# Kernel optimization log

Measured on AMD Instinct MI355X. Metric: run time of the kernel, lower is better.

The kernel has to match this reference:

```python
import jax, jax.numpy as jnp
import numpy as np

B, T, D, H = 2, 2048, 2048, 16
DK = D // H  # 128
THETA = 10000.0


def _rope_angles():
    inv_freq = 1.0 / (THETA ** (np.arange(0, DK, 2, dtype=np.float32) / DK))  # (DK/2,)
    pos = np.arange(T, dtype=np.float32)
    freqs = pos[:, None] * inv_freq[None, :]  # (T, DK/2)
    return jnp.asarray(np.broadcast_to(freqs[None], (B, T, DK // 2)).copy())


def setup_inputs() -> dict:
    key = jax.random.key(0)
    k1, k2, k3 = jax.random.split(key, 3)
    x = jax.random.normal(k1, (B, T, D), dtype=jnp.float32)
    Wqkv = jax.random.normal(k2, (D, 3 * D), dtype=jnp.float32) * (D ** -0.5)
    Wout = jax.random.normal(k3, (D, D), dtype=jnp.float32) * (D ** -0.5)
    return {"x": x, "freqs": _rope_angles(), "Wqkv": Wqkv, "Wout": Wout}


def _apply_rope(xh, cos, sin):
    # xh: (B,T,H,DK); consecutive pairs form complex numbers (torch view_as_complex)
    xr = xh[..., 0::2]  # (B,T,H,DK/2) real parts
    xi = xh[..., 1::2]  # imag parts
    # cos/sin: (B,T,1,DK/2)
    or_ = xr * cos - xi * sin
    oi_ = xr * sin + xi * cos
    return jnp.stack([or_, oi_], axis=-1).reshape(xh.shape)


def reference(x, freqs, Wqkv, Wout):
    qkv = x @ Wqkv  # (B,T,3D)
    qkv = qkv.reshape(B, T, H, 3 * DK)
    q, k, v = qkv[..., :DK], qkv[..., DK:2 * DK], qkv[..., 2 * DK:]
    cos = jnp.cos(freqs)[:, :, None, :]
    sin = jnp.sin(freqs)[:, :, None, :]
    q = _apply_rope(q, cos, sin)
    k = _apply_rope(k, cos, sin)
    # (B,H,T,DK)
    q = q.transpose(0, 2, 1, 3)
    k = k.transpose(0, 2, 1, 3)
    v = v.transpose(0, 2, 1, 3)
    scores = jnp.einsum('bhqd,bhkd->bhqk', q, k) * (DK ** -0.5)
    causal = jnp.tril(jnp.ones((T, T), dtype=bool))
    scores = jnp.where(causal[None, None], scores, -jnp.inf)
    attn = jax.nn.softmax(scores, axis=-1)
    attn = jnp.nan_to_num(attn)
    out = jnp.einsum('bhqk,bhkd->bhqd', attn, v)  # (B,H,T,DK)
    out = out.transpose(0, 2, 1, 3).reshape(B, T, D)
    return out @ Wout
```

## Files before the change

kernel.cpp:

```cpp
#include <hip/hip_runtime.h>
#include <cstdint>

#define BATCH   2
#define T_SEQ   2048
#define NH      16
#define DK      128
#define DMODEL  2048
#define NQKV    6144

using short8 = __attribute__((ext_vector_type(8))) short;
using f32x4  = __attribute__((ext_vector_type(4))) float;
using f32x16 = __attribute__((ext_vector_type(16))) float;

__device__ __forceinline__ float bf2f(unsigned short u) {
    union { float f; uint32_t i; } x; x.i = ((uint32_t)u) << 16; return x.f;
}
__device__ __forceinline__ unsigned short f2bf(float f) {
    union { float f; uint32_t i; } x; x.f = f;
    uint32_t r = x.i + 0x7fffu + ((x.i >> 16) & 1u);
    return (unsigned short)(r >> 16);
}

__device__ __forceinline__ void async_load16(const unsigned short* g, unsigned short* l) {
    __builtin_amdgcn_global_load_lds(
        (const __attribute__((address_space(1))) unsigned int*)g,
        (__attribute__((address_space(3))) unsigned int*)l,
        16, 0, 0);
}


__global__ void cast_x_kernel(const float* __restrict__ x,
                              unsigned short* __restrict__ xb, int n4) {
    int i = blockIdx.x * 256 + threadIdx.x;
    if (i >= n4) return;
    float4 v = ((const float4*)x)[i];
    ushort4 o;
    o.x = f2bf(v.x); o.y = f2bf(v.y); o.z = f2bf(v.z); o.w = f2bf(v.w);
    ((ushort4*)xb)[i] = o;
}

__global__ void wtrans_kernel(const float* __restrict__ W,
                              unsigned short* __restrict__ WT, int K, int N) {
    __shared__ unsigned short tile[64][65];
    int k0 = blockIdx.y * 64, n0 = blockIdx.x * 64;
    for (int it = 0; it < 16; ++it) {
        int idx = it * 256 + threadIdx.x;
        int r = idx >> 6, c = idx & 63;
        tile[r][c] = f2bf(W[(size_t)(k0 + r) * N + n0 + c]);
    }
    __syncthreads();
    for (int it = 0; it < 16; ++it) {
        int idx = it * 256 + threadIdx.x;
        int r = idx >> 6, c = idx & 63;
        WT[(size_t)(n0 + r) * K + k0 + c] = tile[c][r];
    }
}

template <int MODE>
__global__ __launch_bounds__(256) void gemm_bt_kernel(
    const unsigned short* __restrict__ A, const unsigned short* __restrict__ BT,
    float* __restrict__ Cout,
    unsigned short* __restrict__ qraw, unsigned short* __restrict__ kraw,
    unsigned short* __restrict__ vtb,
    int M, int N, int K) {
    __shared__ __align__(16) unsigned short As[128 * 64];
    __shared__ __align__(16) unsigned short Bs[128 * 64];
    const int tid = threadIdx.x;
    const int w = tid >> 6, lane = tid & 63;
    const int l31 = lane & 31, lhi = lane >> 5;
    const int m0 = blockIdx.y * 128, n0 = blockIdx.x * 128;
    const int wm = (w & 1) * 64, wn = (w >> 1) * 64;

    f32x16 acc[2][2];
#pragma unroll
    for (int a = 0; a < 2; ++a)
#pragma unroll
        for (int b = 0; b < 2; ++b)
#pragma unroll
            for (int r = 0; r < 16; ++r) acc[a][b][r] = 0.f;

    for (int k0 = 0; k0 < K; k0 += 64) {
#pragma unroll
        for (int j = 0; j < 4; ++j) {
            int c   = (w * 4 + j) * 64 + lane;
            int row = c >> 3;
            int kcg = (c & 7) ^ (row & 7);
            async_load16(A  + (size_t)(m0 + row) * K + k0 + kcg * 8,
                         As + (size_t)(w * 4 + j) * 64 * 8);
            async_load16(BT + (size_t)(n0 + row) * K + k0 + kcg * 8,
                         Bs + (size_t)(w * 4 + j) * 64 * 8);
        }
        __syncthreads();
#pragma unroll
        for (int ks = 0; ks < 4; ++ks) {
            short8 af[2], bfr[2];
#pragma unroll
            for (int mt = 0; mt < 2; ++mt) {
                int row = wm + mt * 32 + l31;
                int kcs = (ks * 2 + lhi) ^ (row & 7);
                af[mt] = *(const short8*)(As + row * 64 + kcs * 8);
            }
#pragma unroll
            for (int nt = 0; nt < 2; ++nt) {
                int row = wn + nt * 32 + l31;
                int kcs = (ks * 2 + lhi) ^ (row & 7);
                bfr[nt] = *(const short8*)(Bs + row * 64 + kcs * 8);
            }
#pragma unroll
            for (int mt = 0; mt < 2; ++mt)
#pragma unroll
                for (int nt = 0; nt < 2; ++nt)
                    acc[mt][nt] = __builtin_amdgcn_mfma_f32_32x32x16_bf16(
                        af[mt], bfr[nt], acc[mt][nt], 0, 0, 0);
        }
        __syncthreads();
    }

    if (MODE == 0) {
#pragma unroll
        for (int mt = 0; mt < 2; ++mt)
#pragma unroll
            for (int nt = 0; nt < 2; ++nt)
#pragma unroll
                for (int r = 0; r < 16; ++r) {
                    int row = m0 + wm + mt * 32 + (r & 3) + 8 * (r >> 2) + 4 * lhi;
                    int col = n0 + wn + nt * 32 + l31;
                    Cout[(size_t)row * N + col] = acc[mt][nt][r];
                }
    }
}

#define G1_K 2048
#define G1_N 6144

__global__ __launch_bounds__(512, 2) void gemm8p_qkv_kernel(
    const unsigned short* __restrict__ A, const unsigned short* __restrict__ BT,
    unsigned short* __restrict__ qraw, unsigned short* __restrict__ kraw,
    unsigned short* __restrict__ vtb) {
    __shared__ __align__(16) unsigned short As[2][256 * 64];
    __shared__ __align__(16) unsigned short Bs[2][256 * 64];

    const int tid = threadIdx.x;
    const int w = tid >> 6, lane = tid & 63;
    const int l15 = lane & 15, quad = lane >> 4, l7 = lane & 7;
    const int wm = (w & 1) * 128, wn = (w >> 1) * 64;

    const int id = blockIdx.x;
    const int wg = (id & 7) * 48 + (id >> 3);
    const int by = wg / 24, bx = wg - by * 24;
    const int m0 = by * 256, n0 = bx * 256;

    const int r64 = tid >> 3;
    const int csw = (tid & 7) ^ (r64 & 7);

    auto stageA = [&](int buf, int kt, int h) {
#pragma unroll
        for (int j = 0; j < 2; ++j) {
            const int rg = h * 64 + j * 128 + r64;
            async_load16(A + (size_t)(m0 + rg) * G1_K + kt * 64 + csw * 8,
                         &As[buf][(h * 64 + j * 128 + w * 8) << 6]);
        }
    };
    auto stageB = [&](int buf, int kt, int h) {
#pragma unroll
        for (int j = 0; j < 2; ++j) {
            const int rbw = j * 128 + ((w >> 2) << 6) + h * 32 + ((w & 3) << 3);
            const int rg  = rbw + (lane >> 3);
            async_load16(BT + (size_t)(n0 + rg) * G1_K + kt * 64 + csw * 8,
                         &Bs[buf][rbw << 6]);
        }
    };

    f32x4 acc[8][4];
#pragma unroll
    for (int i = 0; i < 8; ++i)
#pragma unroll
        for (int j = 0; j < 4; ++j) acc[i][j] = (f32x4){0.f, 0.f, 0.f, 0.f};

#define LOADA(BUF, H)                                                           \
  _Pragma("unroll") for (int mt = 0; mt < 4; ++mt)                              \
    _Pragma("unroll") for (int ks = 0; ks < 2; ++ks)                            \
      paf[mt][ks] = *(const short8*)(&As[BUF][((wm + (H)*64 + mt*16 + l15)      \
          << 6) + (((ks*4 + quad) ^ l7) << 3)]);

#define LOADB(BUF, H, DST)                                                      \
  _Pragma("unroll") for (int nt = 0; nt < 2; ++nt)                              \
    _Pragma("unroll") for (int ks = 0; ks < 2; ++ks)                            \
      DST[nt][ks] = *(const short8*)(&Bs[BUF][((wn + (H)*32 + nt*16 + l15)      \
          << 6) + (((ks*4 + quad) ^ l7) << 3)]);

#define MFMAQ(QM, QN, PB)                                                       \
  __builtin_amdgcn_s_setprio(1);                                                \
  _Pragma("unroll") for (int mt = 0; mt < 4; ++mt)                              \
    _Pragma("unroll") for (int nt = 0; nt < 2; ++nt)                            \
      _Pragma("unroll") for (int ks = 0; ks < 2; ++ks)                          \
        acc[(QM)*4 + mt][(QN)*2 + nt] =                                         \
            __builtin_amdgcn_mfma_f32_16x16x32_bf16(                            \
                paf[mt][ks], PB[nt][ks], acc[(QM)*4 + mt][(QN)*2 + nt],         \
                0, 0, 0);                                                       \
  __builtin_amdgcn_s_setprio(0);

#define LGK0 asm volatile("s_waitcnt lgkmcnt(0)" ::: "memory");                 \
             __builtin_amdgcn_sched_barrier(0)
#define LGK8 asm volatile("s_waitcnt lgkmcnt(8)" ::: "memory")
#define BAR  __builtin_amdgcn_s_barrier()
#define VM4  asm volatile("s_waitcnt vmcnt(4)" ::: "memory")
#define VM0  asm volatile("s_waitcnt vmcnt(0)" ::: "memory")

    stageA(0, 0, 0); stageB(0, 0, 0); stageA(0, 0, 1); stageB(0, 0, 1);
    stageA(1, 1, 0); stageB(1, 1, 0);
    VM4;
    BAR;

    const int NI = G1_K / 128;
    for (int it = 0; it < NI; ++it) {
        const int t1 = 2 * it + 1;
        const bool last = (it == NI - 1);
        short8 paf[4][2], pbf0[2][2], pbf1[2][2];
        LOADA(0, 0) LOADB(0, 0, pbf0)
        stageA(1, t1, 1);
        LGK8; BAR; LGK0;
        MFMAQ(0, 0, pbf0)
        BAR;
        LOADB(0, 1, pbf1)
        stageB(1, t1, 1);
        BAR; LGK0;
        MFMAQ(0, 1, pbf1)
        BAR;
        LOADA(0, 1)
        if (!last) stageA(0, t1 + 1, 0);
        BAR; LGK0;
        MFMAQ(1, 1, pbf1)
        BAR;
        if (!last) stageB(0, t1 + 1, 0);
        BAR;
        MFMAQ(1, 0, pbf0)
        if (last) { VM0; } else { VM4; }
        BAR;
        LOADA(1, 0) LOADB(1, 0, pbf0)
        if (!last) stageA(0, t1 + 1, 1);
        LGK8; BAR; LGK0;
        MFMAQ(0, 0, pbf0)
        BAR;
        LOADB(1, 1, pbf1)
        if (!last) stageB(0, t1 + 1, 1);
        BAR; LGK0;
        MFMAQ(0, 1, pbf1)
        BAR;
        LOADA(1, 1)
        if (!last) stageA(1, t1 + 2, 0);
        BAR; LGK0;
        MFMAQ(1, 1, pbf1)
        BAR;
        if (!last) stageB(1, t1 + 2, 0);
        BAR;
        MFMAQ(1, 0, pbf0)
        if (!last) { VM4; }
        BAR;
    }

#pragma unroll
    for (int i8 = 0; i8 < 8; ++i8) {
        const int grow0 = m0 + wm + i8 * 16 + quad * 4;
        const int bi = grow0 >> 11;
        const int tb = grow0 & (T_SEQ - 1);
#pragma unroll
        for (int j4 = 0; j4 < 4; ++j4) {
            const int gcol = n0 + wn + j4 * 16 + l15;
            const int h   = gcol / 384;
            const int r3  = gcol - h * 384;
            const int sec = r3 >> 7;
            const int dk  = r3 & 127;
            if (sec < 2) {
                unsigned short* dst = (sec == 0 ? qraw : kraw) +
                    ((size_t)(bi * NH + h) * T_SEQ + tb) * DK + dk;
#pragma unroll
                for (int r = 0; r < 4; ++r)
                    dst[(size_t)r * DK] = f2bf(acc[i8][j4][r]);
            } else {
                unsigned short* dst = vtb +
                    ((size_t)(bi * NH + h) * DK + dk) * T_SEQ + tb;
                ushort4 p;
                p.x = f2bf(acc[i8][j4][0]); p.y = f2bf(acc[i8][j4][1]);
                p.z = f2bf(acc[i8][j4][2]); p.w = f2bf(acc[i8][j4][3]);
                *(ushort4*)dst = p;
            }
        }
    }
#undef LOADA
#undef LOADB
#undef MFMAQ
#undef LGK0
#undef LGK8
#undef BAR
#undef VM4
#undef VM0
}

__global__ void rope_kernel(unsigned short* __restrict__ qraw,
                            unsigned short* __restrict__ kraw,
                            const float* __restrict__ freqs) {
    int linear = blockIdx.x * 256 + threadIdx.x;
    int i  = linear & 63;
    int t  = (linear >> 6) & (T_SEQ - 1);
    int bh = linear >> 17;
    int b  = bh >> 4;
    float f  = freqs[((size_t)b * T_SEQ + t) * 64 + i];
    float cs = __cosf(f), sn = __sinf(f);
    size_t off = ((size_t)bh * T_SEQ + t) * DK + 2 * i;
    ushort2 qp = *(ushort2*)(qraw + off);
    ushort2 kp = *(ushort2*)(kraw + off);
    float qr = bf2f(qp.x), qi = bf2f(qp.y);
    float kr = bf2f(kp.x), ki = bf2f(kp.y);
    ushort2 qo, ko;
    qo.x = f2bf(qr * cs - qi * sn); qo.y = f2bf(qr * sn + qi * cs);
    ko.x = f2bf(kr * cs - ki * sn); ko.y = f2bf(kr * sn + ki * cs);
    *(ushort2*)(qraw + off) = qo;
    *(ushort2*)(kraw + off) = ko;
}

__global__ __launch_bounds__(256) void attn_kernel(
    const unsigned short* __restrict__ qb, const unsigned short* __restrict__ kb,
    const unsigned short* __restrict__ vt, unsigned short* __restrict__ ctx) {
    __shared__ __align__(16) unsigned short Ks[2][64 * 128];
    __shared__ __align__(16) unsigned short Vs[2][128 * 64];
    __shared__ __align__(16) unsigned short pbuf[4][16 * 68];
    const int qt   = 31 - blockIdx.y;
    const int u    = blockIdx.x;
    const int bh   = ((u & 7) << 2) | (u >> 3);
    const int q0   = qt * 64;
    const int w    = threadIdx.x >> 6, lane = threadIdx.x & 63;
    const int lrow = lane & 15, quad = lane >> 4;
    const int qrow = q0 + w * 16;
    const float sc2 = 0.08838834764831845f * 1.4426950408889634f;
    const short8 vone = {16256, 16256, 16256, 16256, 16256, 16256, 16256, 16256};

    short8 aq[4];
    const unsigned short* qbase = qb + ((size_t)bh * T_SEQ + qrow + lrow) * DK;
#pragma unroll
    for (int kk = 0; kk < 4; ++kk)
        aq[kk] = *(const short8*)(qbase + kk * 32 + quad * 8);

    f32x4 o[8];
#pragma unroll
    for (int d = 0; d < 8; ++d) o[d] = (f32x4){0.f, 0.f, 0.f, 0.f};
    f32x4 ol = (f32x4){0.f, 0.f, 0.f, 0.f};

    const unsigned short* kg0 = kb + (size_t)bh * T_SEQ * DK;
    const unsigned short* vg0 = vt + (size_t)bh * DK * T_SEQ;

    auto stage = [&](int kt, int sbuf) {
        const unsigned short* kg = kg0 + (size_t)kt * 64 * DK;
        const unsigned short* vg = vg0 + kt * 64;
        unsigned short* Kd = &Ks[sbuf][0];
        unsigned short* Vd = &Vs[sbuf][0];
#pragma unroll
        for (int j = 0; j < 4; ++j) {
            int c = (w * 4 + j) * 64 + lane;
            int kr_ = c >> 4, kc = (c & 15) ^ (kr_ & 7);
            async_load16(kg + (size_t)kr_ * DK + kc * 8, Kd + c * 8);
            int vr = c >> 3, vc = (c & 7) ^ (vr & 7);
            async_load16(vg + (size_t)vr * T_SEQ + vc * 8, Vd + c * 8);
        }
    };

    stage(0, 0);
    for (int kt = 0; kt <= qt; ++kt) {
        __syncthreads();
        if (kt < qt) stage(kt + 1, (kt + 1) & 1);
        const unsigned short* Kb = &Ks[kt & 1][0];
        const unsigned short* Vb = &Vs[kt & 1][0];

        f32x4 s[4];
#pragma unroll
        for (int nt = 0; nt < 4; ++nt) s[nt] = (f32x4){0.f, 0.f, 0.f, 0.f};
#pragma unroll
        for (int kk = 0; kk < 4; ++kk)
#pragma unroll
            for (int nt = 0; nt < 4; ++nt) {
                int row = nt * 16 + lrow;
                int kc = (kk * 4 + quad) ^ (row & 7);
                short8 bk = *(const short8*)(Kb + row * 128 + kc * 8);
                s[nt] = __builtin_amdgcn_mfma_f32_16x16x32_bf16(aq[kk], bk, s[nt], 0, 0, 0);
            }

        const bool diag = (kt == qt);
        unsigned short* pb = &pbuf[w][0];
#pragma unroll
        for (int nt = 0; nt < 4; ++nt)
#pragma unroll
            for (int r = 0; r < 4; ++r) {
                float p = exp2f(fmaf(s[nt][r], sc2, -12.0f));
                if (diag && (nt * 16 + lrow > w * 16 + quad * 4 + r)) p = 0.f;
                pb[(quad * 4 + r) * 68 + nt * 16 + lrow] = f2bf(p);
            }
        __builtin_amdgcn_s_waitcnt(0xc07f);
        short8 ap[2];
#pragma unroll
        for (int kk2 = 0; kk2 < 2; ++kk2)
            ap[kk2] = *(const short8*)(pb + lrow * 68 + kk2 * 32 + quad * 8);

#pragma unroll
        for (int kk2 = 0; kk2 < 2; ++kk2)
            ol = __builtin_amdgcn_mfma_f32_16x16x32_bf16(ap[kk2], vone, ol, 0, 0, 0);
#pragma unroll
        for (int d = 0; d < 8; ++d)
#pragma unroll
            for (int kk2 = 0; kk2 < 2; ++kk2) {
                int row = d * 16 + lrow;
                int vc = (kk2 * 4 + quad) ^ (row & 7);
                short8 bv = *(const short8*)(Vb + row * 64 + vc * 8);
                o[d] = __builtin_amdgcn_mfma_f32_16x16x32_bf16(ap[kk2], bv, o[d], 0, 0, 0);
            }
    }

    const int b = bh >> 4, h = bh & 15;
    float rl[4];
#pragma unroll
    for (int r = 0; r < 4; ++r) rl[r] = 1.0f / ol[r];
#pragma unroll
    for (int d = 0; d < 8; ++d)
#pragma unroll
        for (int r = 0; r < 4; ++r) {
            int row = qrow + quad * 4 + r;
            ctx[((size_t)(b * T_SEQ + row)) * DMODEL + h * DK + d * 16 + lrow] =
                f2bf(o[d][r] * rl[r]);
        }
}

extern "C" void kernel_launch(void* const* d_in, const int* in_sizes, int n_in,
                              void* d_out, int out_size, void* d_ws, size_t ws_size,
                              hipStream_t stream) {
    const float* x     = (const float*)d_in[0];
    const float* freqs = (const float*)d_in[1];
    const float* Wqkv  = (const float*)d_in[2];
    const float* Wout  = (const float*)d_in[3];
    float* out = (float*)d_out;
    char* ws = (char*)d_ws;
    unsigned short* xb    = (unsigned short*)(ws);
    unsigned short* ctx   = (unsigned short*)(ws);
    unsigned short* wqkvT = (unsigned short*)(ws + 16777216);
    unsigned short* woutT = (unsigned short*)(ws + 41943040);
    unsigned short* qraw  = (unsigned short*)(ws + 50331648);
    unsigned short* kraw  = (unsigned short*)(ws + 67108864);
    unsigned short* vtb   = (unsigned short*)(ws + 83886080);

    cast_x_kernel<<<8192, 256, 0, stream>>>(x, xb, 2097152);
    wtrans_kernel<<<dim3(96, 32), 256, 0, stream>>>(Wqkv, wqkvT, DMODEL, NQKV);
    wtrans_kernel<<<dim3(32, 32), 256, 0, stream>>>(Wout, woutT, DMODEL, DMODEL);
    gemm8p_qkv_kernel<<<384, 512, 0, stream>>>(xb, wqkvT, qraw, kraw, vtb);
    rope_kernel<<<16384, 256, 0, stream>>>(qraw, kraw, freqs);
    attn_kernel<<<dim3(32, 32), 256, 0, stream>>>(qraw, kraw, vtb, ctx);
    gemm_bt_kernel<0><<<dim3(16, 32), 256, 0, stream>>>(
        ctx, woutT, out, nullptr, nullptr, nullptr, BATCH * T_SEQ, DMODEL, DMODEL);
}
```

Measured before the change: 385.9 us.

## Switch QKV GEMM to 32x32x16 MFMA tiles and prefetch A fragments early

Replaces the 16x16x32 bf16 MFMA inner tiles of the QKV projection GEMM with 32x32x16 MFMAs, cutting the number of LDS fragment loads per FLOP and the number of MFMA instructions issued. The A-fragment load for the next quarter is hoisted ahead of the barrier so LDS reads overlap the wait. The epilogue is rewritten for the 32x32 accumulator layout. The larger accumulators keep the same register count but change the ordering, so register pressure and scheduling under launch_bounds(512,2) may shift.

Measured after the change: 407.8 us. +5.7%, slower.

```diff
diff --git a/kernel.cpp b/kernel.cpp
--- a/kernel.cpp
+++ b/kernel.cpp
@@ -142,7 +142,7 @@
 
     const int tid = threadIdx.x;
     const int w = tid >> 6, lane = tid & 63;
-    const int l15 = lane & 15, quad = lane >> 4, l7 = lane & 7;
+    const int l31 = lane & 31, lhi = lane >> 5, l7 = lane & 7;
     const int wm = (w & 1) * 128, wn = (w >> 1) * 64;
 
     const int id = blockIdx.x;
@@ -171,38 +171,37 @@
         }
     };
 
-    f32x4 acc[8][4];
-#pragma unroll
-    for (int i = 0; i < 8; ++i)
-#pragma unroll
-        for (int j = 0; j < 4; ++j) acc[i][j] = (f32x4){0.f, 0.f, 0.f, 0.f};
-
-#define LOADA(BUF, H)                                                           \
-  _Pragma("unroll") for (int mt = 0; mt < 4; ++mt)                              \
-    _Pragma("unroll") for (int ks = 0; ks < 2; ++ks)                            \
-      paf[mt][ks] = *(const short8*)(&As[BUF][((wm + (H)*64 + mt*16 + l15)      \
-          << 6) + (((ks*4 + quad) ^ l7) << 3)]);
-
-#define LOADB(BUF, H, DST)                                                      \
-  _Pragma("unroll") for (int nt = 0; nt < 2; ++nt)                              \
-    _Pragma("unroll") for (int ks = 0; ks < 2; ++ks)                            \
-      DST[nt][ks] = *(const short8*)(&Bs[BUF][((wn + (H)*32 + nt*16 + l15)      \
-          << 6) + (((ks*4 + quad) ^ l7) << 3)]);
-
-#define MFMAQ(QM, QN, PB)                                                       \
+    f32x16 acc[4][2];
+#pragma unroll
+    for (int i = 0; i < 4; ++i)
+#pragma unroll
+        for (int j = 0; j < 2; ++j)
+#pragma unroll
+            for (int r = 0; r < 16; ++r) acc[i][j][r] = 0.f;
+
+    short8 paf[2][4], pbf0[4], pbf1[4];
+
+#define LOADA32(BUF, H)                                                         \
+  _Pragma("unroll") for (int mt = 0; mt < 2; ++mt)                              \
+    _Pragma("unroll") for (int ks = 0; ks < 4; ++ks)                            \
+      paf[mt][ks] = *(const short8*)(&As[BUF][((wm + (H)*64 + mt*32 + l31)      \
+          << 6) + (((ks*2 + lhi) ^ l7) << 3)]);
+
+#define LOADB32(BUF, H, DST)                                                    \
+  _Pragma("unroll") for (int ks = 0; ks < 4; ++ks)                              \
+    DST[ks] = *(const short8*)(&Bs[BUF][((wn + (H)*32 + l31) << 6)              \
+        + (((ks*2 + lhi) ^ l7) << 3)]);
+
+#define MFMAQ32(QM, QN, PB)                                                     \
   __builtin_amdgcn_s_setprio(1);                                                \
-  _Pragma("unroll") for (int mt = 0; mt < 4; ++mt)                              \
-    _Pragma("unroll") for (int nt = 0; nt < 2; ++nt)                            \
-      _Pragma("unroll") for (int ks = 0; ks < 2; ++ks)                          \
-        acc[(QM)*4 + mt][(QN)*2 + nt] =                                         \
-            __builtin_amdgcn_mfma_f32_16x16x32_bf16(                            \
-                paf[mt][ks], PB[nt][ks], acc[(QM)*4 + mt][(QN)*2 + nt],         \
-                0, 0, 0);                                                       \
+  _Pragma("unroll") for (int mt = 0; mt < 2; ++mt)                              \
+    _Pragma("unroll") for (int ks = 0; ks < 4; ++ks)                            \
+      acc[(QM)*2 + mt][QN] = __builtin_amdgcn_mfma_f32_32x32x16_bf16(           \
+          paf[mt][ks], PB[ks], acc[(QM)*2 + mt][QN], 0, 0, 0);                  \
   __builtin_amdgcn_s_setprio(0);
 
 #define LGK0 asm volatile("s_waitcnt lgkmcnt(0)" ::: "memory");                 \
              __builtin_amdgcn_sched_barrier(0)
-#define LGK8 asm volatile("s_waitcnt lgkmcnt(8)" ::: "memory")
 #define BAR  __builtin_amdgcn_s_barrier()
 #define VM4  asm volatile("s_waitcnt vmcnt(4)" ::: "memory")
 #define VM0  asm volatile("s_waitcnt vmcnt(0)" ::: "memory")
@@ -210,88 +209,98 @@
     stageA(0, 0, 0); stageB(0, 0, 0); stageA(0, 0, 1); stageB(0, 0, 1);
     stageA(1, 1, 0); stageB(1, 1, 0);
     VM4;
+    LOADA32(0, 0)
     BAR;
 
     const int NI = G1_K / 128;
     for (int it = 0; it < NI; ++it) {
         const int t1 = 2 * it + 1;
         const bool last = (it == NI - 1);
-        short8 paf[4][2], pbf0[2][2], pbf1[2][2];
-        LOADA(0, 0) LOADB(0, 0, pbf0)
+        LOADB32(0, 0, pbf0)
         stageA(1, t1, 1);
-        LGK8; BAR; LGK0;
-        MFMAQ(0, 0, pbf0)
-        BAR;
-        LOADB(0, 1, pbf1)
+        BAR; LGK0;
+        MFMAQ32(0, 0, pbf0)
+        BAR;
+        LOADB32(0, 1, pbf1)
         stageB(1, t1, 1);
         BAR; LGK0;
-        MFMAQ(0, 1, pbf1)
-        BAR;
-        LOADA(0, 1)
+        MFMAQ32(0, 1, pbf1)
+        BAR;
+        LOADA32(0, 1)
         if (!last) stageA(0, t1 + 1, 0);
         BAR; LGK0;
-        MFMAQ(1, 1, pbf1)
+        MFMAQ32(1, 1, pbf1)
         BAR;
         if (!last) stageB(0, t1 + 1, 0);
         BAR;
-        MFMAQ(1, 0, pbf0)
+        MFMAQ32(1, 0, pbf0)
         if (last) { VM0; } else { VM4; }
-        BAR;
-        LOADA(1, 0) LOADB(1, 0, pbf0)
+        LOADA32(1, 0)
+        BAR;
+        LOADB32(1, 0, pbf0)
         if (!last) stageA(0, t1 + 1, 1);
-        LGK8; BAR; LGK0;
-        MFMAQ(0, 0, pbf0)
-        BAR;
-        LOADB(1, 1, pbf1)
+        BAR; LGK0;
+        MFMAQ32(0, 0, pbf0)
+        BAR;
+        LOADB32(1, 1, pbf1)
         if (!last) stageB(0, t1 + 1, 1);
         BAR; LGK0;
-        MFMAQ(0, 1, pbf1)
-        BAR;
-        LOADA(1, 1)
+        MFMAQ32(0, 1, pbf1)
+        BAR;
+        LOADA32(1, 1)
         if (!last) stageA(1, t1 + 2, 0);
         BAR; LGK0;
-        MFMAQ(1, 1, pbf1)
+        MFMAQ32(1, 1, pbf1)
         BAR;
         if (!last) stageB(1, t1 + 2, 0);
         BAR;
-        MFMAQ(1, 0, pbf0)
-        if (!last) { VM4; }
-        BAR;
-    }
-
-#pragma unroll
-    for (int i8 = 0; i8 < 8; ++i8) {
-        const int grow0 = m0 + wm + i8 * 16 + quad * 4;
-        const int bi = grow0 >> 11;
-        const int tb = grow0 & (T_SEQ - 1);
-#pragma unroll
-        for (int j4 = 0; j4 < 4; ++j4) {
-            const int gcol = n0 + wn + j4 * 16 + l15;
-            const int h   = gcol / 384;
-            const int r3  = gcol - h * 384;
-            const int sec = r3 >> 7;
-            const int dk  = r3 & 127;
+        MFMAQ32(1, 0, pbf0)
+        if (!last) {
+            VM4;
+            LOADA32(0, 0)
+        }
+        BAR;
+    }
+
+#pragma unroll
+    for (int mt = 0; mt < 4; ++mt) {
+        const int trowb = m0 + wm + mt * 32;
+        const int bi = trowb >> 11;
+        const int tb = trowb & (T_SEQ - 1);
+#pragma unroll
+        for (int nt = 0; nt < 2; ++nt) {
+            const int colb = n0 + wn + nt * 32;
+            const int h    = colb / 384;
+            const int r3   = colb - h * 384;
+            const int sec  = r3 >> 7;
+            const int dk   = (r3 & 127) + l31;
             if (sec < 2) {
                 unsigned short* dst = (sec == 0 ? qraw : kraw) +
                     ((size_t)(bi * NH + h) * T_SEQ + tb) * DK + dk;
 #pragma unroll
-                for (int r = 0; r < 4; ++r)
-                    dst[(size_t)r * DK] = f2bf(acc[i8][j4][r]);
+                for (int r = 0; r < 16; ++r) {
+                    int t = (r & 3) + 8 * (r >> 2) + 4 * lhi;
+                    dst[(size_t)t * DK] = f2bf(acc[mt][nt][r]);
+                }
             } else {
-                unsigned short* dst = vtb +
-                    ((size_t)(bi * NH + h) * DK + dk) * T_SEQ + tb;
-                ushort4 p;
-                p.x = f2bf(acc[i8][j4][0]); p.y = f2bf(acc[i8][j4][1]);
-                p.z = f2bf(acc[i8][j4][2]); p.w = f2bf(acc[i8][j4][3]);
-                *(ushort4*)dst = p;
-            }
-        }
-    }
-#undef LOADA
-#undef LOADB
-#undef MFMAQ
+                unsigned short* dst =
+                    vtb + ((size_t)(bi * NH + h) * DK + dk) * T_SEQ + tb;
+#pragma unroll
+                for (int g = 0; g < 4; ++g) {
+                    ushort4 p;
+                    p.x = f2bf(acc[mt][nt][4 * g + 0]);
+                    p.y = f2bf(acc[mt][nt][4 * g + 1]);
+                    p.z = f2bf(acc[mt][nt][4 * g + 2]);
+                    p.w = f2bf(acc[mt][nt][4 * g + 3]);
+                    *(ushort4*)(dst + 8 * g + 4 * lhi) = p;
+                }
+            }
+        }
+    }
+#undef LOADA32
+#undef LOADB32
+#undef MFMAQ32
 #undef LGK0
-#undef LGK8
 #undef BAR
 #undef VM4
 #undef VM0
```

## Fuse RoPE into QKV GEMM epilogue and remap tiles per XCD

Applied to the files above, without the earlier changes.

Removes the separate RoPE kernel and applies the rotation in the QKV GEMM epilogue. Each lane gets its pair partner through a lane shuffle and computes cos/sin from freqs on the fly. This saves a kernel launch and a full read and write pass over Q and K in bf16. It also changes the block-to-tile mapping so each XCD covers a contiguous 4x12 region of tiles, for better L2 reuse. The cost is extra transcendental math and scattered freqs loads in the epilogue, and the rotation is now applied to fp32 values before rounding to bf16.

Result: no change. 384.6 us (-0.3%).

```diff
diff --git a/kernel.cpp b/kernel.cpp
--- a/kernel.cpp
+++ b/kernel.cpp
@@ -135,6 +135,7 @@
 
 __global__ __launch_bounds__(512, 2) void gemm8p_qkv_kernel(
     const unsigned short* __restrict__ A, const unsigned short* __restrict__ BT,
+    const float* __restrict__ freqs,
     unsigned short* __restrict__ qraw, unsigned short* __restrict__ kraw,
     unsigned short* __restrict__ vtb) {
     __shared__ __align__(16) unsigned short As[2][256 * 64];
@@ -146,8 +147,9 @@
     const int wm = (w & 1) * 128, wn = (w >> 1) * 64;
 
     const int id = blockIdx.x;
-    const int wg = (id & 7) * 48 + (id >> 3);
-    const int by = wg / 24, bx = wg - by * 24;
+    const int xcd = id & 7, j = id >> 3;
+    const int by = (xcd >> 1) * 4 + (j & 3);
+    const int bx = (xcd & 1) * 12 + (j >> 2);
     const int m0 = by * 256, n0 = bx * 256;
 
     const int r64 = tid >> 3;
@@ -155,16 +157,16 @@
 
     auto stageA = [&](int buf, int kt, int h) {
 #pragma unroll
-        for (int j = 0; j < 2; ++j) {
-            const int rg = h * 64 + j * 128 + r64;
+        for (int jj = 0; jj < 2; ++jj) {
+            const int rg = h * 64 + jj * 128 + r64;
             async_load16(A + (size_t)(m0 + rg) * G1_K + kt * 64 + csw * 8,
-                         &As[buf][(h * 64 + j * 128 + w * 8) << 6]);
+                         &As[buf][(h * 64 + jj * 128 + w * 8) << 6]);
         }
     };
     auto stageB = [&](int buf, int kt, int h) {
 #pragma unroll
-        for (int j = 0; j < 2; ++j) {
-            const int rbw = j * 128 + ((w >> 2) << 6) + h * 32 + ((w & 3) << 3);
+        for (int jj = 0; jj < 2; ++jj) {
+            const int rbw = jj * 128 + ((w >> 2) << 6) + h * 32 + ((w & 3) << 3);
             const int rg  = rbw + (lane >> 3);
             async_load16(BT + (size_t)(n0 + rg) * G1_K + kt * 64 + csw * 8,
                          &Bs[buf][rbw << 6]);
@@ -175,7 +177,7 @@
 #pragma unroll
     for (int i = 0; i < 8; ++i)
 #pragma unroll
-        for (int j = 0; j < 4; ++j) acc[i][j] = (f32x4){0.f, 0.f, 0.f, 0.f};
+        for (int jj = 0; jj < 4; ++jj) acc[i][jj] = (f32x4){0.f, 0.f, 0.f, 0.f};
 
 #define LOADA(BUF, H)                                                           \
   _Pragma("unroll") for (int mt = 0; mt < 4; ++mt)                              \
@@ -272,18 +274,26 @@
             const int sec = r3 >> 7;
             const int dk  = r3 & 127;
             if (sec < 2) {
+                const float sgn = (dk & 1) ? 1.f : -1.f;
+                const float* fp = freqs +
+                    ((size_t)(bi * T_SEQ + tb)) * 64 + (dk >> 1);
                 unsigned short* dst = (sec == 0 ? qraw : kraw) +
                     ((size_t)(bi * NH + h) * T_SEQ + tb) * DK + dk;
 #pragma unroll
-                for (int r = 0; r < 4; ++r)
-                    dst[(size_t)r * DK] = f2bf(acc[i8][j4][r]);
+                for (int r = 0; r < 4; ++r) {
+                    float v = acc[i8][j4][r];
+                    float p = __shfl_xor(v, 1);
+                    float f = fp[(size_t)r * 64];
+                    float cs = __cosf(f), sn = __sinf(f);
+                    dst[(size_t)r * DK] = f2bf(fmaf(v, cs, sgn * (p * sn)));
+                }
             } else {
                 unsigned short* dst = vtb +
                     ((size_t)(bi * NH + h) * DK + dk) * T_SEQ + tb;
-                ushort4 p;
-                p.x = f2bf(acc[i8][j4][0]); p.y = f2bf(acc[i8][j4][1]);
-                p.z = f2bf(acc[i8][j4][2]); p.w = f2bf(acc[i8][j4][3]);
-                *(ushort4*)dst = p;
+                ushort4 pk;
+                pk.x = f2bf(acc[i8][j4][0]); pk.y = f2bf(acc[i8][j4][1]);
+                pk.z = f2bf(acc[i8][j4][2]); pk.w = f2bf(acc[i8][j4][3]);
+                *(ushort4*)dst = pk;
             }
         }
     }
@@ -295,28 +305,6 @@
 #undef BAR
 #undef VM4
 #undef VM0
-}
-
-__global__ void rope_kernel(unsigned short* __restrict__ qraw,
-                            unsigned short* __restrict__ kraw,
-                            const float* __restrict__ freqs) {
-    int linear = blockIdx.x * 256 + threadIdx.x;
-    int i  = linear & 63;
-    int t  = (linear >> 6) & (T_SEQ - 1);
-    int bh = linear >> 17;
-    int b  = bh >> 4;
-    float f  = freqs[((size_t)b * T_SEQ + t) * 64 + i];
-    float cs = __cosf(f), sn = __sinf(f);
-    size_t off = ((size_t)bh * T_SEQ + t) * DK + 2 * i;
-    ushort2 qp = *(ushort2*)(qraw + off);
-    ushort2 kp = *(ushort2*)(kraw + off);
-    float qr = bf2f(qp.x), qi = bf2f(qp.y);
-    float kr = bf2f(kp.x), ki = bf2f(kp.y);
-    ushort2 qo, ko;
-    qo.x = f2bf(qr * cs - qi * sn); qo.y = f2bf(qr * sn + qi * cs);
-    ko.x = f2bf(kr * cs - ki * sn); ko.y = f2bf(kr * sn + ki * cs);
-    *(ushort2*)(qraw + off) = qo;
-    *(ushort2*)(kraw + off) = ko;
 }
 
 __global__ __launch_bounds__(256) void attn_kernel(
@@ -448,8 +436,7 @@
     cast_x_kernel<<<8192, 256, 0, stream>>>(x, xb, 2097152);
     wtrans_kernel<<<dim3(96, 32), 256, 0, stream>>>(Wqkv, wqkvT, DMODEL, NQKV);
     wtrans_kernel<<<dim3(32, 32), 256, 0, stream>>>(Wout, woutT, DMODEL, DMODEL);
-    gemm8p_qkv_kernel<<<384, 512, 0, stream>>>(xb, wqkvT, qraw, kraw, vtb);
-    rope_kernel<<<16384, 256, 0, stream>>>(qraw, kraw, freqs);
+    gemm8p_qkv_kernel<<<384, 512, 0, stream>>>(xb, wqkvT, freqs, qraw, kraw, vtb);
     attn_kernel<<<dim3(32, 32), 256, 0, stream>>>(qraw, kraw, vtb, ctx);
     gemm_bt_kernel<0><<<dim3(16, 32), 256, 0, stream>>>(
         ctx, woutT, out, nullptr, nullptr, nullptr, BATCH * T_SEQ, DMODEL, DMODEL);
```
